# Kernel tuning notes

Hardware: AMD Instinct MI355X
Metric: run time of the kernel (lower is better)

## Reference

```python
import jax, jax.numpy as jnp
import numpy as np

B, N, E = 1, 2048, 2048
HQ, HK = 32, 8          # query heads, kv heads
D = E // HQ             # per-query-head dim = 64
G = HQ // HK            # groups per kv head = 4
KV_E = HK * D           # kv_embed_dim = 512
EHK = E // HK           # G output dim per kv head = 256 = G*D


def setup_inputs() -> dict:
    key = jax.random.key(0)
    ks = jax.random.split(key, 14)
    s = 0.02
    f32 = jnp.float32
    return {
        "q": jax.random.normal(ks[0], (B, N, E), f32),
        "k": jax.random.normal(ks[1], (B, N, E), f32),
        "v": jax.random.normal(ks[2], (B, N, E), f32),
        "Wq": jax.random.normal(ks[3], (E, KV_E), f32) * s,
        "bq": jax.random.normal(ks[4], (KV_E,), f32) * s,
        "Wk": jax.random.normal(ks[5], (E, KV_E), f32) * s,
        "bk": jax.random.normal(ks[6], (KV_E,), f32) * s,
        "Wv": jax.random.normal(ks[7], (E, KV_E), f32) * s,
        "bv": jax.random.normal(ks[8], (KV_E,), f32) * s,
        "WG": jax.random.normal(ks[9], (HK, D, EHK), f32) * s,  # per-kv-head Linear(D -> G*D)
        "bG": jax.random.normal(ks[10], (HK, EHK), f32) * s,
        "Wfc": jax.random.normal(ks[11], (E, E), f32) * s,
        "bfc": jax.random.normal(ks[12], (E,), f32) * s,
    }


def reference(q, k, v, Wq, bq, Wk, bk, Wv, bv, WG, bG, Wfc, bfc):
    b, n, _ = q.shape
    # projections to kv_embed_dim
    Q = q @ Wq + bq                                   # [b,n,HK*D]
    K = k @ Wk + bk
    V = v @ Wv + bv
    # per-kv-head compound transform G[i]: D -> G*D
    Q = Q.reshape(b, n, HK, D)
    Q = jnp.einsum('bnhd,hde->bnhe', Q, WG) + bG      # [b,n,HK,G*D]
    # 'b n h (g d) -> b n (h g) d' then 'b (h g) n d -> b g h n d'
    Qg = Q.reshape(b, n, HK, G, D).transpose(0, 3, 2, 1, 4)   # [b,g,h,n,d]
    Kh = K.reshape(b, n, HK, D).transpose(0, 2, 1, 3)         # [b,h,s,d]
    Vh = V.reshape(b, n, HK, D).transpose(0, 2, 1, 3)
    scores = jnp.einsum('bghnd,bhsd->bghns', Qg, Kh)
    # causal mask applied BEFORE dividing by scale (faithful to source, incl.
    # the source's scale direction: softmax(scores / d**-0.5))
    mask = jnp.tril(jnp.ones((n, n), dtype=bool))
    scores = jnp.where(mask[None, None, None], scores, jnp.finfo(scores.dtype).min)
    scale = D ** (-0.5)
    attn = jax.nn.softmax(scores / scale, axis=-1)
    out = jnp.einsum('bghns,bhsd->bghnd', attn, Vh)
    # 'b g h n d -> b n (h g) d' -> 'b n (h d)'
    out = out.transpose(0, 3, 2, 1, 4).reshape(b, n, E)
    return out @ Wfc + bfc
```

## Files before the change

### kernel.cpp

```cpp
#include <hip/hip_runtime.h>
#include <hip/hip_bf16.h>

using bf16 = __hip_bfloat16;
typedef __attribute__((ext_vector_type(8))) short short8;
typedef __attribute__((ext_vector_type(4))) float f32x4;
typedef __attribute__((ext_vector_type(16))) float f32x16;
typedef __attribute__((ext_vector_type(4))) unsigned u32x4;
typedef __attribute__((ext_vector_type(4))) short s16x4;

#define DEVI static __device__ __forceinline__

DEVI short8 ld8(const void* p) { return *(const short8*)p; }
DEVI void st8(void* p, short8 v) { *(short8*)p = v; }

DEVI f32x4 mfma16(short8 a, short8 b, f32x4 c) {
  return __builtin_amdgcn_mfma_f32_16x16x32_bf16(a, b, c, 0, 0, 0);
}
DEVI f32x16 mfma32(short8 a, short8 b, f32x16 c) {
  return __builtin_amdgcn_mfma_f32_32x32x16_bf16(a, b, c, 0, 0, 0);
}
DEVI unsigned pk2(float a, float b) {
  unsigned short ua = __builtin_bit_cast(unsigned short, __float2bfloat16(a));
  unsigned short ub = __builtin_bit_cast(unsigned short, __float2bfloat16(b));
  return (unsigned)ua | ((unsigned)ub << 16);
}
DEVI int swz(int row, int colb) { return row * 128 + (colb ^ ((row & 7) << 4)); }

__global__ void detect_k(const void* __restrict__ qsrc, int* __restrict__ flag) {
  if (threadIdx.x == 0 && blockIdx.x == 0) {
    const unsigned short* u = (const unsigned short*)qsrc;
    int c = 0;
    for (int i = 0; i < 256; ++i) {
      int e = (u[i] >> 7) & 0xFF;
      if (e > 140 || e < 90) ++c;
    }
    *flag = (c >= 16) ? 1 : 0;
  }
}

__global__ void convert3_k(const void* __restrict__ s0, const void* __restrict__ s1,
                           const void* __restrict__ s2, bf16* __restrict__ d0,
                           bf16* __restrict__ d1, bf16* __restrict__ d2, int n,
                           const int* __restrict__ flag) {
  int z = blockIdx.z;
  const void* src = z == 0 ? s0 : z == 1 ? s1 : s2;
  bf16* dst = z == 0 ? d0 : z == 1 ? d1 : d2;
  int f = *flag;
  int i0 = (blockIdx.x * blockDim.x + threadIdx.x) * 8;
  int stride = gridDim.x * blockDim.x * 8;
  if (f) {
    const float* s = (const float*)src;
    for (int i = i0; i < n; i += stride) {
      bf16 tmp[8];
#pragma unroll
      for (int j = 0; j < 8; ++j) tmp[j] = __float2bfloat16(s[i + j]);
      st8(dst + i, *(short8*)tmp);
    }
  } else {
    const bf16* s = (const bf16*)src;
    for (int i = i0; i < n; i += stride) st8(dst + i, ld8(s + i));
  }
}

__global__ void convert5_k(const void* b0, const void* b1, const void* b2,
                           const void* b3, const void* b4,
                           bf16* __restrict__ dst, const int* __restrict__ flag) {
  int f = *flag;
  const void* srcs[5] = {b0, b1, b2, b3, b4};
  const int sz[5] = {512, 512, 512, 2048, 2048};
  const int off[5] = {0, 512, 1024, 1536, 3584};
  for (int j = 0; j < 5; ++j)
    for (int i = threadIdx.x; i < sz[j]; i += blockDim.x)
      dst[off[j] + i] = f ? __float2bfloat16(((const float*)srcs[j])[i])
                          : ((const bf16*)srcs[j])[i];
}

__global__ void transpose_cvt_k(const void* __restrict__ src, bf16* __restrict__ dst,
                                int R, int C, const int* __restrict__ flag) {
  int f = *flag;
  __shared__ bf16 t[32][33];
  size_t base = (size_t)blockIdx.z * R * C;
  int c0 = blockIdx.x * 32, r0 = blockIdx.y * 32;
  int tx = threadIdx.x, ty = threadIdx.y;
  size_t si = base + (size_t)(r0 + ty) * C + (c0 + tx);
  t[ty][tx] = f ? __float2bfloat16(((const float*)src)[si]) : ((const bf16*)src)[si];
  __syncthreads();
  dst[base + (size_t)(c0 + ty) * R + (r0 + tx)] = t[tx][ty];
}

__global__ void transpose_w3_k(const void* __restrict__ w0, const void* __restrict__ w1,
                               const void* __restrict__ w2, bf16* __restrict__ dst,
                               const int* __restrict__ flag) {
  int f = *flag;
  int sel = blockIdx.z;
  const void* src = sel == 0 ? w0 : sel == 1 ? w1 : w2;
  bf16* d = dst + (size_t)sel * 512 * 2048;
  __shared__ bf16 t[32][33];
  int c0 = blockIdx.x * 32, r0 = blockIdx.y * 32;
  int tx = threadIdx.x, ty = threadIdx.y;
  size_t si = (size_t)(r0 + ty) * 512 + (c0 + tx);
  t[ty][tx] = f ? __float2bfloat16(((const float*)src)[si]) : ((const bf16*)src)[si];
  __syncthreads();
  d[(size_t)(c0 + ty) * 2048 + (r0 + tx)] = t[tx][ty];
}

DEVI void gemm128(const bf16* A, const bf16* Bt, int lda, int ldb, int K,
                  bf16* ldsA, bf16* ldsB, f32x4 (&acc)[4][4]) {
  const int t = threadIdx.x, w = t >> 6, lane = t & 63;
  const int wm = (w >> 1) * 64, wn = (w & 1) * 64;
  const int r = lane & 15, kb = (lane >> 4) * 8;
  const int flat0 = t * 16, flat1 = 4096 + t * 16;
  const int row0 = flat0 >> 6, cb0 = flat0 & 63;
  const int row1 = flat1 >> 6, cb1 = flat1 & 63;
  for (int k0 = 0; k0 < K; k0 += 32) {
    short8 a0 = ld8((const char*)A + (size_t)row0 * lda * 2 + (size_t)k0 * 2 + cb0);
    short8 a1 = ld8((const char*)A + (size_t)row1 * lda * 2 + (size_t)k0 * 2 + cb1);
    short8 b0 = ld8((const char*)Bt + (size_t)row0 * ldb * 2 + (size_t)k0 * 2 + cb0);
    short8 b1 = ld8((const char*)Bt + (size_t)row1 * ldb * 2 + (size_t)k0 * 2 + cb1);
    __syncthreads();
    st8((char*)ldsA + flat0, a0);
    st8((char*)ldsA + flat1, a1);
    st8((char*)ldsB + flat0, b0);
    st8((char*)ldsB + flat1, b1);
    __syncthreads();
    short8 af[4], bfv[4];
#pragma unroll
    for (int mi = 0; mi < 4; ++mi)
      af[mi] = ld8(ldsA + (wm + mi * 16 + r) * 32 + kb);
#pragma unroll
    for (int ni = 0; ni < 4; ++ni)
      bfv[ni] = ld8(ldsB + (wn + ni * 16 + r) * 32 + kb);
#pragma unroll
    for (int mi = 0; mi < 4; ++mi)
#pragma unroll
      for (int ni = 0; ni < 4; ++ni)
        acc[mi][ni] = mfma16(af[mi], bfv[ni], acc[mi][ni]);
  }
}

__global__ __launch_bounds__(256) void qkv_k(
    const bf16* __restrict__ q, const bf16* __restrict__ k, const bf16* __restrict__ v,
    const bf16* __restrict__ WT, const bf16* __restrict__ biasN,
    bf16* __restrict__ Q0, bf16* __restrict__ Kb, bf16* __restrict__ VTb) {
  __shared__ bf16 ldsA[128 * 32];
  __shared__ bf16 ldsB[128 * 32];
  int m0 = blockIdx.x * 128;
  int bc = blockIdx.y, sel = bc >> 2, n0 = (bc & 3) * 128;
  const bf16* A = sel == 0 ? q : sel == 1 ? k : v;
  const bf16* bias = biasN + sel * 512;
  const bf16* Bt = WT + (size_t)sel * 512 * 2048 + (size_t)n0 * 2048;
  f32x4 acc[4][4];
  f32x4 z = {0.f, 0.f, 0.f, 0.f};
#pragma unroll
  for (int mi = 0; mi < 4; ++mi)
#pragma unroll
    for (int ni = 0; ni < 4; ++ni) acc[mi][ni] = z;
  gemm128(A + (size_t)m0 * 2048, Bt, 2048, 2048, 2048, ldsA, ldsB, acc);
  const int t = threadIdx.x, w = t >> 6, lane = t & 63;
  const int wm = (w >> 1) * 64, wn = (w & 1) * 64;
#pragma unroll
  for (int mi = 0; mi < 4; ++mi)
#pragma unroll
    for (int ni = 0; ni < 4; ++ni)
#pragma unroll
      for (int i = 0; i < 4; ++i) {
        int row = m0 + wm + mi * 16 + ((lane >> 4) * 4 + i);
        int ch = n0 + wn + ni * 16 + (lane & 15);
        float val = acc[mi][ni][i] + __bfloat162float(bias[ch]);
        bf16 o = __float2bfloat16(val);
        if (sel == 0)      Q0[(size_t)row * 512 + ch] = o;
        else if (sel == 1) Kb[((size_t)(ch >> 6) * 2048 + row) * 64 + (ch & 63)] = o;
        else               VTb[((size_t)(ch >> 6) * 64 + (ch & 63)) * 2048 + row] = o;
      }
}

__global__ __launch_bounds__(256) void gtrans_k(
    const bf16* __restrict__ Q0, const bf16* __restrict__ WGT,
    const bf16* __restrict__ bGN, bf16* __restrict__ QG) {
  __shared__ bf16 Wlds[256 * 64];
  __shared__ bf16 Qlds[64 * 64];
  int n0 = blockIdx.x * 64, h = blockIdx.y;
  int t = threadIdx.x, w = t >> 6, lane = t & 63;
  const char* wsrc = (const char*)(WGT + (size_t)h * 256 * 64);
  short8 wreg[8], qreg[2];
#pragma unroll
  for (int it = 0; it < 8; ++it)
    wreg[it] = ld8(wsrc + it * 4096 + t * 16);
#pragma unroll
  for (int it = 0; it < 2; ++it) {
    int flat = it * 4096 + t * 16;
    int row = flat >> 7, cb = flat & 127;
    qreg[it] = ld8((const char*)Q0 + (size_t)(n0 + row) * 1024 + h * 128 + cb);
  }
#pragma unroll
  for (int it = 0; it < 8; ++it)
    st8((char*)Wlds + it * 4096 + t * 16, wreg[it]);
#pragma unroll
  for (int it = 0; it < 2; ++it)
    st8((char*)Qlds + it * 4096 + t * 16, qreg[it]);
  __syncthreads();
  int r = lane & 15, kb = (lane >> 4) * 8;
  short8 af0 = ld8(Qlds + (w * 16 + r) * 64 + kb);
  short8 af1 = ld8(Qlds + (w * 16 + r) * 64 + 32 + kb);
#pragma unroll
  for (int ni = 0; ni < 16; ++ni) {
    f32x4 a = {0.f, 0.f, 0.f, 0.f};
    a = mfma16(af0, ld8(Wlds + (ni * 16 + r) * 64 + kb), a);
    a = mfma16(af1, ld8(Wlds + (ni * 16 + r) * 64 + 32 + kb), a);
    int e = ni * 16 + r;
    int g = e >> 6, d = e & 63;
    float bias = __bfloat162float(bGN[h * 256 + e]);
#pragma unroll
    for (int i = 0; i < 4; ++i) {
      int row = n0 + w * 16 + (lane >> 4) * 4 + i;
      QG[((size_t)(g * 8 + h) * 2048 + row) * 64 + d] =
          __float2bfloat16((a[i] + bias) * 8.0f);
    }
  }
}

__global__ __launch_bounds__(256) void attn_k(
    const bf16* __restrict__ QG, const bf16* __restrict__ Kb,
    const bf16* __restrict__ VTb, bf16* __restrict__ AO) {
  __shared__ bf16 Klds[2][64 * 64];
  __shared__ bf16 Vlds[2][64 * 64];
  int q0 = (gridDim.x - 1 - blockIdx.x) * 128;
  int hh = blockIdx.y, g = hh >> 3, h = hh & 7;
  int t = threadIdx.x, w = t >> 6, lane = t & 63;
  int qq = lane & 31, hp = lane >> 5;
  const char* Khb = (const char*)(Kb + (size_t)h * 2048 * 64);
  const char* Vhb = (const char*)(VTb + (size_t)h * 64 * 2048);
  const bf16* Qh = QG + (size_t)hh * 2048 * 64;
  int qrow = q0 + w * 32 + qq;
  int qmin = q0 + w * 32;

  short8 qf[4];
#pragma unroll
  for (int kc = 0; kc < 4; ++kc)
    qf[kc] = ld8(Qh + (size_t)qrow * 64 + kc * 16 + hp * 8);

  int srow = t >> 3;
  int scolb = (t & 7) * 16;
  int soff = swz(srow, scolb);
  int soff2 = swz(srow + 32, scolb);

  f32x16 acc[2];
#pragma unroll
  for (int i = 0; i < 16; ++i) { acc[0][i] = 0.f; acc[1][i] = 0.f; }
  float m_run = -1e30f, l_run = 0.f;

  int nt = q0 / 64 + 2;
  {
    short8 k0 = ld8(Khb + (size_t)srow * 128 + scolb);
    short8 k1 = ld8(Khb + (size_t)(srow + 32) * 128 + scolb);
    short8 v0 = ld8(Vhb + (size_t)srow * 4096 + scolb);
    short8 v1 = ld8(Vhb + (size_t)(srow + 32) * 4096 + scolb);
    st8((char*)Klds[0] + soff, k0);
    st8((char*)Klds[0] + soff2, k1);
    st8((char*)Vlds[0] + soff, v0);
    st8((char*)Vlds[0] + soff2, v1);
  }
  for (int tt = 0; tt < nt; ++tt) {
    int cur = tt & 1;
    int s0 = tt * 64;
    __syncthreads();
    bool have_next = (tt + 1 < nt);
    short8 nk0, nk1, nv0, nv1;
    if (have_next) {
      int sn = s0 + 64;
      nk0 = ld8(Khb + (size_t)(sn + srow) * 128 + scolb);
      nk1 = ld8(Khb + (size_t)(sn + srow + 32) * 128 + scolb);
      nv0 = ld8(Vhb + (size_t)srow * 4096 + sn * 2 + scolb);
      nv1 = ld8(Vhb + (size_t)(srow + 32) * 4096 + sn * 2 + scolb);
    }
    if (s0 <= qmin + 31) {
      const char* Kc = (const char*)Klds[cur];
      const char* Vc = (const char*)Vlds[cur];
      f32x16 sa0, sa1;
#pragma unroll
      for (int i = 0; i < 16; ++i) { sa0[i] = 0.f; sa1[i] = 0.f; }
#pragma unroll
      for (int kc = 0; kc < 4; ++kc) {
        short8 kf0 = ld8(Kc + swz(qq, kc * 32 + hp * 16));
        short8 kf1 = ld8(Kc + swz(32 + qq, kc * 32 + hp * 16));
        sa0 = mfma32(kf0, qf[kc], sa0);
        sa1 = mfma32(kf1, qf[kc], sa1);
      }
      if (s0 + 63 > qmin) {
#pragma unroll
        for (int rg = 0; rg < 16; ++rg) {
          int sr = s0 + (rg & 3) + 8 * (rg >> 2) + 4 * hp;
          if (sr > qrow) sa0[rg] = -1e30f;
          if (sr + 32 > qrow) sa1[rg] = -1e30f;
        }
      }
      float tmax = sa0[0];
#pragma unroll
      for (int rg = 1; rg < 16; ++rg) tmax = fmaxf(tmax, sa0[rg]);
#pragma unroll
      for (int rg = 0; rg < 16; ++rg) tmax = fmaxf(tmax, sa1[rg]);
      tmax = fmaxf(tmax, __shfl_xor(tmax, 32));
      float mnew = fmaxf(m_run, tmax);
      float alpha = __expf(m_run - mnew);
      m_run = mnew;
      float rs = 0.f;
#pragma unroll
      for (int rg = 0; rg < 16; ++rg) { sa0[rg] = __expf(sa0[rg] - mnew); rs += sa0[rg]; }
#pragma unroll
      for (int rg = 0; rg < 16; ++rg) { sa1[rg] = __expf(sa1[rg] - mnew); rs += sa1[rg]; }
      rs += __shfl_xor(rs, 32);
      l_run = l_run * alpha + rs;
#pragma unroll
      for (int i = 0; i < 16; ++i) { acc[0][i] *= alpha; acc[1][i] *= alpha; }
      unsigned wpk0[8], wpk1[8];
#pragma unroll
      for (int rp = 0; rp < 8; ++rp) {
        wpk0[rp] = pk2(sa0[2 * rp], sa0[2 * rp + 1]);
        wpk1[rp] = pk2(sa1[2 * rp], sa1[2 * rp + 1]);
      }
#pragma unroll
      for (int kc = 0; kc < 4; ++kc) {
        const unsigned* wp = (kc < 2) ? wpk0 : wpk1;
        int base = (kc & 1) * 4;
        unsigned own0 = wp[base + 0], own1 = wp[base + 1];
        unsigned own2 = wp[base + 2], own3 = wp[base + 3];
        unsigned send0 = hp ? own0 : own2;
        unsigned send1 = hp ? own1 : own3;
        unsigned r0 = (unsigned)__shfl_xor((int)send0, 32);
        unsigned r1 = (unsigned)__shfl_xor((int)send1, 32);
        u32x4 pv;
        pv[0] = hp ? r0 : own0;
        pv[1] = hp ? r1 : own1;
        pv[2] = hp ? own2 : r0;
        pv[3] = hp ? own3 : r1;
        short8 pa = __builtin_bit_cast(short8, pv);
        short8 vf0 = ld8(Vc + swz(qq, kc * 32 + hp * 16));
        short8 vf1 = ld8(Vc + swz(32 + qq, kc * 32 + hp * 16));
        acc[0] = mfma32(vf0, pa, acc[0]);
        acc[1] = mfma32(vf1, pa, acc[1]);
      }
    }
    if (have_next) {
      int nb = cur ^ 1;
      st8((char*)Klds[nb] + soff, nk0);
      st8((char*)Klds[nb] + soff2, nk1);
      st8((char*)Vlds[nb] + soff, nv0);
      st8((char*)Vlds[nb] + soff2, nv1);
    }
  }
  float rli = 1.0f / l_run;
  bf16* aob = AO + (size_t)qrow * 2048 + h * 256 + g * 64;
#pragma unroll
  for (int ds = 0; ds < 2; ++ds)
#pragma unroll
    for (int rq = 0; rq < 4; ++rq) {
      s16x4 o4;
#pragma unroll
      for (int i = 0; i < 4; ++i)
        o4[i] = __builtin_bit_cast(short, __float2bfloat16(acc[ds][rq * 4 + i] * rli));
      int d0 = ds * 32 + 8 * rq + 4 * hp;
      *(s16x4*)(aob + d0) = o4;
    }
}

__global__ __launch_bounds__(256) void outproj_k(
    const bf16* __restrict__ AO, const bf16* __restrict__ WfcT,
    const bf16* __restrict__ bfcN, void* __restrict__ outv,
    const int* __restrict__ flag) {
  __shared__ bf16 ldsA[128 * 32];
  __shared__ bf16 ldsB[128 * 32];
  int f = *flag;
  int m0 = blockIdx.x * 128, n0 = blockIdx.y * 128;
  f32x4 acc[4][4];
  f32x4 z = {0.f, 0.f, 0.f, 0.f};
#pragma unroll
  for (int mi = 0; mi < 4; ++mi)
#pragma unroll
    for (int ni = 0; ni < 4; ++ni) acc[mi][ni] = z;
  gemm128(AO + (size_t)m0 * 2048, WfcT + (size_t)n0 * 2048, 2048, 2048, 2048,
          ldsA, ldsB, acc);
  const int t = threadIdx.x, w = t >> 6, lane = t & 63;
  const int wm = (w >> 1) * 64, wn = (w & 1) * 64;
#pragma unroll
  for (int mi = 0; mi < 4; ++mi)
#pragma unroll
    for (int ni = 0; ni < 4; ++ni)
#pragma unroll
      for (int i = 0; i < 4; ++i) {
        int row = m0 + wm + mi * 16 + ((lane >> 4) * 4 + i);
        int ch = n0 + wn + ni * 16 + (lane & 15);
        float val = acc[mi][ni][i] + __bfloat162float(bfcN[ch]);
        size_t idx = (size_t)row * 2048 + ch;
        if (f) ((float*)outv)[idx] = val;
        else   ((bf16*)outv)[idx] = __float2bfloat16(val);
      }
}

extern "C" void kernel_launch(void* const* d_in, const int* in_sizes, int n_in,
                              void* d_out, int out_size, void* d_ws, size_t ws_size,
                              hipStream_t stream) {
  const void* q   = d_in[0];
  const void* k   = d_in[1];
  const void* v   = d_in[2];
  const void* Wq  = d_in[3];
  const void* bq  = d_in[4];
  const void* Wk  = d_in[5];
  const void* bk  = d_in[6];
  const void* Wv  = d_in[7];
  const void* bv  = d_in[8];
  const void* WG  = d_in[9];
  const void* bG  = d_in[10];
  const void* Wfc = d_in[11];
  const void* bfc = d_in[12];

  bf16* ws = (bf16*)d_ws;
  int* flag = (int*)d_ws;
  bf16* biasN = ws + 32;
  bf16* WT    = ws + 6144;
  bf16* WGT   = ws + 3151872;
  bf16* Q0    = ws + 3282944;
  bf16* Kb    = ws + 4331520;
  bf16* VTb   = ws + 5380096;
  bf16* R1    = ws + 6428672;
  bf16* R2    = ws + 10622976;
  bf16* R3    = ws + 14817280;
  bf16* qn = R1; bf16* QG = R1;
  bf16* kn = R2; bf16* AO = R2;
  bf16* vn = R3; bf16* WfcT = R3;
  bf16* bGN = biasN + 1536, *bfcN = biasN + 3584;

  detect_k<<<1, 64, 0, stream>>>(q, flag);
  convert3_k<<<dim3(1024, 1, 3), 256, 0, stream>>>(q, k, v, qn, kn, vn, 4194304, flag);
  convert5_k<<<1, 256, 0, stream>>>(bq, bk, bv, bG, bfc, biasN, flag);

  dim3 b32(32, 32, 1);
  transpose_w3_k<<<dim3(16, 64, 3), b32, 0, stream>>>(Wq, Wk, Wv, WT, flag);
  transpose_cvt_k<<<dim3(8, 2, 8), b32, 0, stream>>>(WG, WGT, 64, 256, flag);

  qkv_k<<<dim3(16, 12, 1), 256, 0, stream>>>(qn, kn, vn, WT, biasN, Q0, Kb, VTb);
  gtrans_k<<<dim3(32, 8, 1), 256, 0, stream>>>(Q0, WGT, bGN, QG);
  attn_k<<<dim3(16, 32, 1), 256, 0, stream>>>(QG, Kb, VTb, AO);
  transpose_cvt_k<<<dim3(64, 64, 1), b32, 0, stream>>>(Wfc, WfcT, 2048, 2048, flag);
  outproj_k<<<dim3(16, 16, 1), 256, 0, stream>>>(AO, WfcT, bfcN, d_out, flag);
}
```

Before: 329.5 us.

## Pre-swizzle K/V into MFMA fragment layout and drop LDS staging in attention

The QKV projection now writes K and V directly into a fragment-ordered layout, so the attention kernel loads its MFMA operands straight from global memory. This removes LDS staging, swizzling and block barriers, and walks 32-key tiles per wave, each wave stopping at its own causal bound. It also adds a lazy softmax rescale that only rescales when the running max grows by more than a threshold, and switches GEMM and gtrans LDS fills to global_load_lds async copies. In exchange, K and V fragments are re-read from global or L2 by every wave with no LDS reuse.

```diff
diff --git a/kernel.cpp b/kernel.cpp
--- a/kernel.cpp
+++ b/kernel.cpp
@@ -13,6 +13,12 @@
 DEVI short8 ld8(const void* p) { return *(const short8*)p; }
 DEVI void st8(void* p, short8 v) { *(short8*)p = v; }
 
+DEVI void async_load16(const void* g, void* lds) {
+  __builtin_amdgcn_global_load_lds(
+      (__attribute__((address_space(1))) void*)g,
+      (__attribute__((address_space(3))) void*)lds, 16, 0, 0);
+}
+
 DEVI f32x4 mfma16(short8 a, short8 b, f32x4 c) {
   return __builtin_amdgcn_mfma_f32_16x16x32_bf16(a, b, c, 0, 0, 0);
 }
@@ -24,7 +30,6 @@
   unsigned short ub = __builtin_bit_cast(unsigned short, __float2bfloat16(b));
   return (unsigned)ua | ((unsigned)ub << 16);
 }
-DEVI int swz(int row, int colb) { return row * 128 + (colb ^ ((row & 7) << 4)); }
 
 __global__ void detect_k(const void* __restrict__ qsrc, int* __restrict__ flag) {
   if (threadIdx.x == 0 && blockIdx.x == 0) {
@@ -109,19 +114,17 @@
   const int t = threadIdx.x, w = t >> 6, lane = t & 63;
   const int wm = (w >> 1) * 64, wn = (w & 1) * 64;
   const int r = lane & 15, kb = (lane >> 4) * 8;
-  const int flat0 = t * 16, flat1 = 4096 + t * 16;
-  const int row0 = flat0 >> 6, cb0 = flat0 & 63;
-  const int row1 = flat1 >> 6, cb1 = flat1 & 63;
   for (int k0 = 0; k0 < K; k0 += 32) {
-    short8 a0 = ld8((const char*)A + (size_t)row0 * lda * 2 + (size_t)k0 * 2 + cb0);
-    short8 a1 = ld8((const char*)A + (size_t)row1 * lda * 2 + (size_t)k0 * 2 + cb1);
-    short8 b0 = ld8((const char*)Bt + (size_t)row0 * ldb * 2 + (size_t)k0 * 2 + cb0);
-    short8 b1 = ld8((const char*)Bt + (size_t)row1 * ldb * 2 + (size_t)k0 * 2 + cb1);
     __syncthreads();
-    st8((char*)ldsA + flat0, a0);
-    st8((char*)ldsA + flat1, a1);
-    st8((char*)ldsB + flat0, b0);
-    st8((char*)ldsB + flat1, b1);
+#pragma unroll
+    for (int it = 0; it < 2; ++it) {
+      int flat = it * 4096 + t * 16;
+      int row = flat >> 6, cb = flat & 63;
+      async_load16((const char*)A + (size_t)row * lda * 2 + (size_t)k0 * 2 + cb,
+                   (char*)ldsA + it * 4096 + w * 1024);
+      async_load16((const char*)Bt + (size_t)row * ldb * 2 + (size_t)k0 * 2 + cb,
+                   (char*)ldsB + it * 4096 + w * 1024);
+    }
     __syncthreads();
     short8 af[4], bfv[4];
 #pragma unroll
@@ -141,7 +144,7 @@
 __global__ __launch_bounds__(256) void qkv_k(
     const bf16* __restrict__ q, const bf16* __restrict__ k, const bf16* __restrict__ v,
     const bf16* __restrict__ WT, const bf16* __restrict__ biasN,
-    bf16* __restrict__ Q0, bf16* __restrict__ Kb, bf16* __restrict__ VTb) {
+    bf16* __restrict__ Q0, bf16* __restrict__ KF, bf16* __restrict__ VF) {
   __shared__ bf16 ldsA[128 * 32];
   __shared__ bf16 ldsB[128 * 32];
   int m0 = blockIdx.x * 128;
@@ -168,9 +171,19 @@
         int ch = n0 + wn + ni * 16 + (lane & 15);
         float val = acc[mi][ni][i] + __bfloat162float(bias[ch]);
         bf16 o = __float2bfloat16(val);
-        if (sel == 0)      Q0[(size_t)row * 512 + ch] = o;
-        else if (sel == 1) Kb[((size_t)(ch >> 6) * 2048 + row) * 64 + (ch & 63)] = o;
-        else               VTb[((size_t)(ch >> 6) * 64 + (ch & 63)) * 2048 + row] = o;
+        if (sel == 0) {
+          Q0[(size_t)row * 512 + ch] = o;
+        } else if (sel == 1) {
+          int h = ch >> 6, d = ch & 63;
+          int tt = row >> 5, qq2 = row & 31;
+          int kc = d >> 4, hp2 = (d >> 3) & 1, j = d & 7;
+          KF[((((size_t)(h * 64 + tt) * 4 + kc) * 2 + hp2) * 32 + qq2) * 8 + j] = o;
+        } else {
+          int h = ch >> 6, d = ch & 63;
+          int tt = row >> 5, c = (row >> 4) & 1, hp2 = (row >> 3) & 1, j = row & 7;
+          int dh = d >> 5, qq2 = d & 31;
+          VF[(((((size_t)(h * 64 + tt) * 2 + c) * 2 + dh) * 64) + hp2 * 32 + qq2) * 8 + j] = o;
+        }
       }
 }
 
@@ -182,22 +195,16 @@
   int n0 = blockIdx.x * 64, h = blockIdx.y;
   int t = threadIdx.x, w = t >> 6, lane = t & 63;
   const char* wsrc = (const char*)(WGT + (size_t)h * 256 * 64);
-  short8 wreg[8], qreg[2];
 #pragma unroll
   for (int it = 0; it < 8; ++it)
-    wreg[it] = ld8(wsrc + it * 4096 + t * 16);
+    async_load16(wsrc + it * 4096 + t * 16, (char*)Wlds + it * 4096 + w * 1024);
 #pragma unroll
   for (int it = 0; it < 2; ++it) {
     int flat = it * 4096 + t * 16;
     int row = flat >> 7, cb = flat & 127;
-    qreg[it] = ld8((const char*)Q0 + (size_t)(n0 + row) * 1024 + h * 128 + cb);
-  }
-#pragma unroll
-  for (int it = 0; it < 8; ++it)
-    st8((char*)Wlds + it * 4096 + t * 16, wreg[it]);
-#pragma unroll
-  for (int it = 0; it < 2; ++it)
-    st8((char*)Qlds + it * 4096 + t * 16, qreg[it]);
+    async_load16((const char*)Q0 + (size_t)(n0 + row) * 1024 + h * 128 + cb,
+                 (char*)Qlds + it * 4096 + w * 1024);
+  }
   __syncthreads();
   int r = lane & 15, kb = (lane >> 4) * 8;
   short8 af0 = ld8(Qlds + (w * 16 + r) * 64 + kb);
@@ -220,16 +227,14 @@
 }
 
 __global__ __launch_bounds__(256) void attn_k(
-    const bf16* __restrict__ QG, const bf16* __restrict__ Kb,
-    const bf16* __restrict__ VTb, bf16* __restrict__ AO) {
-  __shared__ bf16 Klds[2][64 * 64];
-  __shared__ bf16 Vlds[2][64 * 64];
+    const bf16* __restrict__ QG, const bf16* __restrict__ KF,
+    const bf16* __restrict__ VF, bf16* __restrict__ AO) {
   int q0 = (gridDim.x - 1 - blockIdx.x) * 128;
   int hh = blockIdx.y, g = hh >> 3, h = hh & 7;
   int t = threadIdx.x, w = t >> 6, lane = t & 63;
   int qq = lane & 31, hp = lane >> 5;
-  const char* Khb = (const char*)(Kb + (size_t)h * 2048 * 64);
-  const char* Vhb = (const char*)(VTb + (size_t)h * 64 * 2048);
+  const bf16* KFh = KF + (size_t)h * 131072;
+  const bf16* VFh = VF + (size_t)h * 131072;
   const bf16* Qh = QG + (size_t)hh * 2048 * 64;
   int qrow = q0 + w * 32 + qq;
   int qmin = q0 + w * 32;
@@ -239,113 +244,82 @@
   for (int kc = 0; kc < 4; ++kc)
     qf[kc] = ld8(Qh + (size_t)qrow * 64 + kc * 16 + hp * 8);
 
-  int srow = t >> 3;
-  int scolb = (t & 7) * 16;
-  int soff = swz(srow, scolb);
-  int soff2 = swz(srow + 32, scolb);
-
   f32x16 acc[2];
 #pragma unroll
   for (int i = 0; i < 16; ++i) { acc[0][i] = 0.f; acc[1][i] = 0.f; }
   float m_run = -1e30f, l_run = 0.f;
 
-  int nt = q0 / 64 + 2;
-  {
-    short8 k0 = ld8(Khb + (size_t)srow * 128 + scolb);
-    short8 k1 = ld8(Khb + (size_t)(srow + 32) * 128 + scolb);
-    short8 v0 = ld8(Vhb + (size_t)srow * 4096 + scolb);
-    short8 v1 = ld8(Vhb + (size_t)(srow + 32) * 4096 + scolb);
-    st8((char*)Klds[0] + soff, k0);
-    st8((char*)Klds[0] + soff2, k1);
-    st8((char*)Vlds[0] + soff, v0);
-    st8((char*)Vlds[0] + soff2, v1);
-  }
-  for (int tt = 0; tt < nt; ++tt) {
-    int cur = tt & 1;
-    int s0 = tt * 64;
-    __syncthreads();
-    bool have_next = (tt + 1 < nt);
-    short8 nk0, nk1, nv0, nv1;
-    if (have_next) {
-      int sn = s0 + 64;
-      nk0 = ld8(Khb + (size_t)(sn + srow) * 128 + scolb);
-      nk1 = ld8(Khb + (size_t)(sn + srow + 32) * 128 + scolb);
-      nv0 = ld8(Vhb + (size_t)srow * 4096 + sn * 2 + scolb);
-      nv1 = ld8(Vhb + (size_t)(srow + 32) * 4096 + sn * 2 + scolb);
-    }
-    if (s0 <= qmin + 31) {
-      const char* Kc = (const char*)Klds[cur];
-      const char* Vc = (const char*)Vlds[cur];
-      f32x16 sa0, sa1;
-#pragma unroll
-      for (int i = 0; i < 16; ++i) { sa0[i] = 0.f; sa1[i] = 0.f; }
-#pragma unroll
-      for (int kc = 0; kc < 4; ++kc) {
-        short8 kf0 = ld8(Kc + swz(qq, kc * 32 + hp * 16));
-        short8 kf1 = ld8(Kc + swz(32 + qq, kc * 32 + hp * 16));
-        sa0 = mfma32(kf0, qf[kc], sa0);
-        sa1 = mfma32(kf1, qf[kc], sa1);
+  short8 kf[4], knx[4];
+#pragma unroll
+  for (int kc = 0; kc < 4; ++kc)
+    kf[kc] = ld8(KFh + ((size_t)kc * 64 + lane) * 8);
+
+  int tlast = qmin >> 5;
+  for (int t2 = 0; t2 <= tlast; ++t2) {
+    bool hn = t2 < tlast;
+    if (hn) {
+#pragma unroll
+      for (int kc = 0; kc < 4; ++kc)
+        knx[kc] = ld8(KFh + (((size_t)(t2 + 1) * 4 + kc) * 64 + lane) * 8);
+    }
+    f32x16 sa;
+#pragma unroll
+    for (int i = 0; i < 16; ++i) sa[i] = 0.f;
+#pragma unroll
+    for (int kc = 0; kc < 4; ++kc) sa = mfma32(kf[kc], qf[kc], sa);
+    if (t2 == tlast) {
+#pragma unroll
+      for (int rg = 0; rg < 16; ++rg) {
+        int sr = t2 * 32 + (rg & 3) + 8 * (rg >> 2) + 4 * hp;
+        if (sr > qrow) sa[rg] = -1e30f;
       }
-      if (s0 + 63 > qmin) {
-#pragma unroll
-        for (int rg = 0; rg < 16; ++rg) {
-          int sr = s0 + (rg & 3) + 8 * (rg >> 2) + 4 * hp;
-          if (sr > qrow) sa0[rg] = -1e30f;
-          if (sr + 32 > qrow) sa1[rg] = -1e30f;
-        }
-      }
-      float tmax = sa0[0];
-#pragma unroll
-      for (int rg = 1; rg < 16; ++rg) tmax = fmaxf(tmax, sa0[rg]);
-#pragma unroll
-      for (int rg = 0; rg < 16; ++rg) tmax = fmaxf(tmax, sa1[rg]);
-      tmax = fmaxf(tmax, __shfl_xor(tmax, 32));
+    }
+    float tmax = sa[0];
+#pragma unroll
+    for (int rg = 1; rg < 16; ++rg) tmax = fmaxf(tmax, sa[rg]);
+    tmax = fmaxf(tmax, __shfl_xor(tmax, 32));
+    if (!__all(tmax <= m_run + 8.0f)) {
       float mnew = fmaxf(m_run, tmax);
       float alpha = __expf(m_run - mnew);
       m_run = mnew;
-      float rs = 0.f;
-#pragma unroll
-      for (int rg = 0; rg < 16; ++rg) { sa0[rg] = __expf(sa0[rg] - mnew); rs += sa0[rg]; }
-#pragma unroll
-      for (int rg = 0; rg < 16; ++rg) { sa1[rg] = __expf(sa1[rg] - mnew); rs += sa1[rg]; }
-      rs += __shfl_xor(rs, 32);
-      l_run = l_run * alpha + rs;
+      l_run *= alpha;
 #pragma unroll
       for (int i = 0; i < 16; ++i) { acc[0][i] *= alpha; acc[1][i] *= alpha; }
-      unsigned wpk0[8], wpk1[8];
-#pragma unroll
-      for (int rp = 0; rp < 8; ++rp) {
-        wpk0[rp] = pk2(sa0[2 * rp], sa0[2 * rp + 1]);
-        wpk1[rp] = pk2(sa1[2 * rp], sa1[2 * rp + 1]);
-      }
-#pragma unroll
-      for (int kc = 0; kc < 4; ++kc) {
-        const unsigned* wp = (kc < 2) ? wpk0 : wpk1;
-        int base = (kc & 1) * 4;
-        unsigned own0 = wp[base + 0], own1 = wp[base + 1];
-        unsigned own2 = wp[base + 2], own3 = wp[base + 3];
-        unsigned send0 = hp ? own0 : own2;
-        unsigned send1 = hp ? own1 : own3;
-        unsigned r0 = (unsigned)__shfl_xor((int)send0, 32);
-        unsigned r1 = (unsigned)__shfl_xor((int)send1, 32);
-        u32x4 pv;
-        pv[0] = hp ? r0 : own0;
-        pv[1] = hp ? r1 : own1;
-        pv[2] = hp ? own2 : r0;
-        pv[3] = hp ? own3 : r1;
-        short8 pa = __builtin_bit_cast(short8, pv);
-        short8 vf0 = ld8(Vc + swz(qq, kc * 32 + hp * 16));
-        short8 vf1 = ld8(Vc + swz(32 + qq, kc * 32 + hp * 16));
-        acc[0] = mfma32(vf0, pa, acc[0]);
-        acc[1] = mfma32(vf1, pa, acc[1]);
-      }
-    }
-    if (have_next) {
-      int nb = cur ^ 1;
-      st8((char*)Klds[nb] + soff, nk0);
-      st8((char*)Klds[nb] + soff2, nk1);
-      st8((char*)Vlds[nb] + soff, nv0);
-      st8((char*)Vlds[nb] + soff2, nv1);
+    }
+    float rs = 0.f;
+#pragma unroll
+    for (int rg = 0; rg < 16; ++rg) {
+      float p = __expf(sa[rg] - m_run);
+      sa[rg] = p;
+      rs += p;
+    }
+    rs += __shfl_xor(rs, 32);
+    l_run += rs;
+    unsigned wpk[8];
+#pragma unroll
+    for (int rp = 0; rp < 8; ++rp) wpk[rp] = pk2(sa[2 * rp], sa[2 * rp + 1]);
+#pragma unroll
+    for (int c = 0; c < 2; ++c) {
+      unsigned own0 = wpk[c * 4 + 0], own1 = wpk[c * 4 + 1];
+      unsigned own2 = wpk[c * 4 + 2], own3 = wpk[c * 4 + 3];
+      unsigned send0 = hp ? own0 : own2;
+      unsigned send1 = hp ? own1 : own3;
+      unsigned r0 = (unsigned)__shfl_xor((int)send0, 32);
+      unsigned r1 = (unsigned)__shfl_xor((int)send1, 32);
+      u32x4 pv;
+      pv[0] = hp ? r0 : own0;
+      pv[1] = hp ? r1 : own1;
+      pv[2] = hp ? own2 : r0;
+      pv[3] = hp ? own3 : r1;
+      short8 pa = __builtin_bit_cast(short8, pv);
+      short8 vf0 = ld8(VFh + ((((size_t)t2 * 2 + c) * 2 + 0) * 64 + lane) * 8);
+      short8 vf1 = ld8(VFh + ((((size_t)t2 * 2 + c) * 2 + 1) * 64 + lane) * 8);
+      acc[0] = mfma32(vf0, pa, acc[0]);
+      acc[1] = mfma32(vf1, pa, acc[1]);
+    }
+    if (hn) {
+#pragma unroll
+      for (int kc = 0; kc < 4; ++kc) kf[kc] = knx[kc];
     }
   }
   float rli = 1.0f / l_run;
@@ -419,8 +393,8 @@
   bf16* WT    = ws + 6144;
   bf16* WGT   = ws + 3151872;
   bf16* Q0    = ws + 3282944;
-  bf16* Kb    = ws + 4331520;
-  bf16* VTb   = ws + 5380096;
+  bf16* KF    = ws + 4331520;
+  bf16* VF    = ws + 5380096;
   bf16* R1    = ws + 6428672;
   bf16* R2    = ws + 10622976;
   bf16* R3    = ws + 14817280;
@@ -437,9 +411,9 @@
   transpose_w3_k<<<dim3(16, 64, 3), b32, 0, stream>>>(Wq, Wk, Wv, WT, flag);
   transpose_cvt_k<<<dim3(8, 2, 8), b32, 0, stream>>>(WG, WGT, 64, 256, flag);
 
-  qkv_k<<<dim3(16, 12, 1), 256, 0, stream>>>(qn, kn, vn, WT, biasN, Q0, Kb, VTb);
+  qkv_k<<<dim3(16, 12, 1), 256, 0, stream>>>(qn, kn, vn, WT, biasN, Q0, KF, VF);
   gtrans_k<<<dim3(32, 8, 1), 256, 0, stream>>>(Q0, WGT, bGN, QG);
-  attn_k<<<dim3(16, 32, 1), 256, 0, stream>>>(QG, Kb, VTb, AO);
+  attn_k<<<dim3(16, 32, 1), 256, 0, stream>>>(QG, KF, VF, AO);
   transpose_cvt_k<<<dim3(64, 64, 1), b32, 0, stream>>>(Wfc, WfcT, 2048, 2048, flag);
   outproj_k<<<dim3(16, 16, 1), 256, 0, stream>>>(AO, WfcT, bfcN, d_out, flag);
 }
```

New measurement: 316.7 us. -3.9%, faster.
